# Performance work log

Hardware: AMD Instinct MI355X
Metric: run time of the kernel (lower is better)

## Reference

```python
import jax, jax.numpy as jnp
import numpy as np

NUM_SEQS = 4
SEQ_LEN = 2048
T = NUM_SEQS * SEQ_LEN          # total tokens
D_IN = 4096
D_OUT = 4096
NUM_ADAPTERS = 8
MAX_RANK = 64
CACHE_LEN = NUM_ADAPTERS * MAX_RANK  # 512 pages


def setup_inputs() -> dict:
    key = jax.random.key(0)
    ks = jax.random.split(key, 8)
    x = jax.random.normal(ks[0], (T, D_IN), dtype=jnp.float32)
    weight = jax.random.normal(ks[1], (D_OUT, D_IN), dtype=jnp.float32) * 0.02
    bias = jax.random.normal(ks[2], (D_OUT,), dtype=jnp.float32) * 0.02
    a_cache = jax.random.normal(ks[3], (CACHE_LEN, D_IN), dtype=jnp.float32) * 0.02
    b_cache = jax.random.normal(ks[4], (CACHE_LEN, D_OUT), dtype=jnp.float32) * 0.02
    b_start_loc = (jnp.arange(NUM_SEQS) * SEQ_LEN).astype(jnp.int32)
    b_adapter_ids = jax.random.randint(ks[5], (NUM_SEQS,), 0, NUM_ADAPTERS).astype(jnp.int32)
    b_scaling = jax.random.uniform(ks[6], (NUM_SEQS,), dtype=jnp.float32, minval=0.5, maxval=2.0)
    # page i for (adapter a, rank slot r) lives at a*MAX_RANK + r
    rank_page_table = jnp.arange(CACHE_LEN, dtype=jnp.int32).reshape(NUM_ADAPTERS, MAX_RANK)
    ranks = jax.random.randint(ks[7], (NUM_ADAPTERS,), 1, MAX_RANK + 1).astype(jnp.int32)
    return {"x": x, "weight": weight, "bias": bias, "a_cache": a_cache,
            "b_cache": b_cache, "b_start_loc": b_start_loc,
            "b_adapter_ids": b_adapter_ids, "b_scaling": b_scaling,
            "rank_page_table": rank_page_table, "ranks": ranks}


def reference(x, weight, bias, a_cache, b_cache, b_start_loc,
              b_adapter_ids, b_scaling, rank_page_table, ranks):
    t = x.shape[0]
    num_adapters, max_rank = rank_page_table.shape
    # map each token to its sequence -> adapter id / scaling (mbgmm dispatch)
    seg = jnp.searchsorted(b_start_loc, jnp.arange(t, dtype=b_start_loc.dtype),
                           side='right') - 1                      # [T]
    tok_adapter = b_adapter_ids[seg]                              # [T]
    tok_scale = b_scaling[seg]                                    # [T]
    # gather paged LoRA A/B weights per adapter: [A, R, D]
    A_all = a_cache[rank_page_table]                              # [A, R, D_in]
    B_all = b_cache[rank_page_table]                              # [A, R, D_out]
    # mbgmm_a: xa[t, r] = x[t] . A[adapter(t), r], zero beyond rank
    xa_all = jnp.einsum('td,ard->tar', x, A_all)                  # [T, A, R]
    rmask = (jnp.arange(max_rank)[None, :] < ranks[:, None])      # [A, R]
    onehot = (tok_adapter[:, None] == jnp.arange(num_adapters)[None, :])  # [T, A]
    sel = (onehot[:, :, None] & rmask[None, :, :]).astype(x.dtype)  # [T, A, R]
    xa_sel = xa_all * sel
    # mbgmm_b: lora_out[t] = scaling * sum_r xa[t, r] * B[adapter(t), r]
    lora_out = jnp.einsum('tar,aro->to', xa_sel, B_all) * tok_scale[:, None]
    base_out = x @ weight.T + bias
    return base_out + lora_out
```

## Files before the change

kernel.cpp:

```cpp
#include <hip/hip_runtime.h>
#include <hip/hip_bf16.h>

typedef unsigned short u16;
typedef unsigned int u32;
typedef __attribute__((ext_vector_type(8))) short bf16x8;
typedef __attribute__((ext_vector_type(4))) float f32x4;

#define T_TOK 8192
#define DIN 4096
#define DOUT 4096
#define N_SEQS 4
#define N_ADPT 8
#define MAXR 64
#define CACHE_LEN 512

__device__ __forceinline__ u16 f2bf(float f) {
    u32 u = __builtin_bit_cast(u32, f);
    u += 0x7fffu + ((u >> 16) & 1u);
    return (u16)(u >> 16);
}

__device__ __forceinline__ void load_lds16(const u16* g, u16* l) {
    __builtin_amdgcn_global_load_lds(
        (const __attribute__((address_space(1))) u32*)g,
        (__attribute__((address_space(3))) u32*)l, 16, 0, 0);
}

__global__ void cvt_all(const float* __restrict__ x, const float* __restrict__ w,
                        const float* __restrict__ a,
                        u16* __restrict__ xb, u16* __restrict__ wb, u16* __restrict__ ab) {
    const int n_x = T_TOK * DIN / 4, n_w = DOUT * DIN / 4, n_a = CACHE_LEN * DIN / 4;
    int i = blockIdx.x * 256 + threadIdx.x;
    int stride = gridDim.x * 256;
    for (int j = i; j < n_x + n_w + n_a; j += stride) {
        const float* src; u16* dst; int k;
        if (j < n_x)            { src = x; dst = xb; k = j; }
        else if (j < n_x + n_w) { src = w; dst = wb; k = j - n_x; }
        else                    { src = a; dst = ab; k = j - n_x - n_w; }
        float4 v = reinterpret_cast<const float4*>(src)[k];
        ushort4 o;
        o.x = f2bf(v.x); o.y = f2bf(v.y); o.z = f2bf(v.z); o.w = f2bf(v.w);
        reinterpret_cast<ushort4*>(dst)[k] = o;
    }
}

__global__ void build_bt(const float* __restrict__ b_cache, const int* __restrict__ rpt,
                         u16* __restrict__ Bt) {
    int id = blockIdx.x * 256 + threadIdx.x;
    int n  = id & (DOUT - 1);
    int rb = (id >> 12) & 7;
    int a  = id >> 15;
    union { u16 u[8]; uint4 v; } pack;
    #pragma unroll
    for (int j = 0; j < 8; ++j) {
        int r = rb * 8 + j;
        int page = rpt[a * MAXR + r];
        pack.u[j] = f2bf(b_cache[(long)page * DOUT + n]);
    }
    *reinterpret_cast<uint4*>(&Bt[((long)(a * DOUT + n)) * MAXR + rb * 8]) = pack.v;
}

__launch_bounds__(256)
__global__ void xa_kernel(const u16* __restrict__ xb, const u16* __restrict__ ab,
                          const int* __restrict__ b_start_loc,
                          const int* __restrict__ b_adapter_ids,
                          const int* __restrict__ rpt,
                          float* __restrict__ xa_part) {
    int tblk = blockIdx.x >> 2, kseg = blockIdx.x & 3;
    int t0 = tblk * 128;
    int seg = 0;
    #pragma unroll
    for (int i = 1; i < N_SEQS; ++i) if (b_start_loc[i] <= t0) seg = i;
    int adapter = b_adapter_ids[seg];

    __shared__ __attribute__((aligned(16))) u16 As[2 * 4096];
    __shared__ __attribute__((aligned(16))) u16 Bs[2 * 2048];

    int tid = threadIdx.x;
    int lane = tid & 63, wave = tid >> 6;
    int lr = lane & 15, lk = lane >> 4;

    int e0 = wave * 64 + lane;
    int e1 = 256 + e0;
    int ra0 = e0 >> 2, ca0 = (e0 & 3) * 8;
    int ra1 = e1 >> 2, ca1 = (e1 & 3) * 8;
    const u16* gA0 = xb + (long)(t0 + ra0) * DIN + kseg * 1024 + ca0;
    const u16* gA1 = xb + (long)(t0 + ra1) * DIN + kseg * 1024 + ca1;
    int page = rpt[adapter * MAXR + ra0];
    const u16* gB = ab + (long)page * DIN + kseg * 1024 + ca0;

    f32x4 acc[2][4] = {};

    #define XSTAGE(s, buf)                                                         \
        do {                                                                       \
            load_lds16(gA0 + (s) * 32, As + (buf) * 4096 + wave * 512);            \
            load_lds16(gA1 + (s) * 32, As + (buf) * 4096 + 2048 + wave * 512);     \
            load_lds16(gB + (s) * 32,  Bs + (buf) * 2048 + wave * 512);            \
        } while (0)

    XSTAGE(0, 0);
    for (int s = 0; s < 32; ++s) {
        int b = s & 1;
        if (s < 31) {
            XSTAGE(s + 1, b ^ 1);
            asm volatile("s_waitcnt vmcnt(3)" ::: "memory");
        } else {
            asm volatile("s_waitcnt vmcnt(0)" ::: "memory");
        }
        __builtin_amdgcn_s_barrier();
        __builtin_amdgcn_sched_barrier(0);

        bf16x8 af[2], bfr[4];
        #pragma unroll
        for (int m = 0; m < 2; ++m)
            af[m] = *(const bf16x8*)&As[b * 4096 + (wave * 32 + m * 16 + lr) * 32 + lk * 8];
        #pragma unroll
        for (int n = 0; n < 4; ++n)
            bfr[n] = *(const bf16x8*)&Bs[b * 2048 + (n * 16 + lr) * 32 + lk * 8];
        #pragma unroll
        for (int m = 0; m < 2; ++m)
            #pragma unroll
            for (int n = 0; n < 4; ++n)
                acc[m][n] = __builtin_amdgcn_mfma_f32_16x16x32_bf16(af[m], bfr[n], acc[m][n], 0, 0, 0);

        __builtin_amdgcn_s_barrier();
        __builtin_amdgcn_sched_barrier(0);
    }
    #undef XSTAGE

    float* dst = xa_part + (long)kseg * T_TOK * MAXR;
    #pragma unroll
    for (int m = 0; m < 2; ++m) {
        int trow = t0 + wave * 32 + m * 16 + lk * 4;
        #pragma unroll
        for (int n = 0; n < 4; ++n) {
            int r = n * 16 + lr;
            #pragma unroll
            for (int j = 0; j < 4; ++j)
                dst[(long)(trow + j) * MAXR + r] = acc[m][n][j];
        }
    }
}

__global__ void xa_fin(const float* __restrict__ xa_part,
                       const int* __restrict__ b_start_loc,
                       const int* __restrict__ b_adapter_ids,
                       const float* __restrict__ b_scaling,
                       const int* __restrict__ ranks,
                       u16* __restrict__ xa) {
    const int N = T_TOK * MAXR;
    int i = blockIdx.x * 256 + threadIdx.x;
    if (i >= N) return;
    int t = i >> 6, r = i & 63;
    int seg = 0;
    #pragma unroll
    for (int s = 1; s < N_SEQS; ++s) if (b_start_loc[s] <= t) seg = s;
    int adapter = b_adapter_ids[seg];
    float v = xa_part[i] + xa_part[N + i] + xa_part[2 * N + i] + xa_part[3 * N + i];
    v = (r < ranks[adapter]) ? v * b_scaling[seg] : 0.0f;
    xa[i] = f2bf(v);
}

__launch_bounds__(512, 2)
__global__ void gemm256_kernel(const u16* __restrict__ xb, const u16* __restrict__ wb,
                               const float* __restrict__ bias,
                               const u16* __restrict__ xa, const u16* __restrict__ Bt,
                               const int* __restrict__ b_start_loc,
                               const int* __restrict__ b_adapter_ids,
                               float* __restrict__ out) {
    __shared__ __attribute__((aligned(16))) u16 lds[32768];

    int bid = blockIdx.x;
    int wgid = (bid & 7) * 64 + (bid >> 3);
    int mt = wgid >> 4, nt = wgid & 15;
    int brow = mt * 256, bcol = nt * 256;

    int seg = 0;
    #pragma unroll
    for (int i = 1; i < N_SEQS; ++i) if (b_start_loc[i] <= brow) seg = i;
    int adapter = b_adapter_ids[seg];

    int tid = threadIdx.x;
    int lane = tid & 63, wave = tid >> 6;
    int wm = wave >> 2, wn = wave & 3;
    int lr = lane & 15, lk = lane >> 4;

    int lsw = (tid & 7) ^ ((tid >> 3) & 7);
    int c8  = (lsw & 3) * 8;
    int r0  = (tid >> 3) * 2 + (lsw >> 2);
    const long odA0 = (long)(brow + r0) * DIN + c8;
    const long odA1 = odA0 + 128L * DIN;
    const long odB0 = (long)(bcol + r0) * DIN + c8;
    const long odB1 = odB0 + 128L * DIN;
    const long o6A0 = (long)(brow + r0) * MAXR + c8;
    const long o6A1 = o6A0 + 128L * MAXR;
    const long o6B0 = (long)(adapter * DOUT + bcol + r0) * MAXR + c8;
    const long o6B1 = o6B0 + 128L * MAXR;

    #define STAGE(T, buf)                                                          \
        do {                                                                       \
            u16* dA = lds + (buf) * 8192 + tid * 8;                                \
            u16* dB = lds + 16384 + (buf) * 8192 + tid * 8;                        \
            if ((T) < 128) {                                                       \
                long ko = (long)(T) * 32;                                          \
                load_lds16(xb + odA0 + ko, dA);                                    \
                load_lds16(xb + odA1 + ko, dA + 4096);                             \
                load_lds16(wb + odB0 + ko, dB);                                    \
                load_lds16(wb + odB1 + ko, dB + 4096);                             \
            } else {                                                               \
                long ko = (long)((T) - 128) * 32;                                  \
                load_lds16(xa + o6A0 + ko, dA);                                    \
                load_lds16(xa + o6A1 + ko, dA + 4096);                             \
                load_lds16(Bt + o6B0 + ko, dB);                                    \
                load_lds16(Bt + o6B1 + ko, dB + 4096);                             \
            }                                                                      \
        } while (0)

    const int laneByte = (lr >> 1) * 128 + 16 * ((((lr & 1) << 2) + lk) ^ (lr >> 1));
    const char* ldsc = (const char*)lds;
    const int cA = wm * 8192 + laneByte;
    const int cB = 32768 + wn * 4096 + laneByte;

    #define READF(FA, FB, par)                                                     \
        do {                                                                       \
            const char* pA = ldsc + (par) * 16384 + cA;                            \
            const char* pB = ldsc + (par) * 16384 + cB;                            \
            _Pragma("unroll")                                                      \
            for (int ni = 0; ni < 4; ++ni) FB[ni] = *(const bf16x8*)(pB + ni * 1024); \
            _Pragma("unroll")                                                      \
            for (int mi = 0; mi < 8; ++mi) FA[mi] = *(const bf16x8*)(pA + mi * 1024); \
        } while (0)

    #define MFMA32(FA, FB)                                                         \
        do {                                                                       \
            _Pragma("unroll")                                                      \
            for (int mi = 0; mi < 8; ++mi)                                         \
                _Pragma("unroll")                                                  \
                for (int ni = 0; ni < 4; ++ni)                                     \
                    acc[mi][ni] = __builtin_amdgcn_mfma_f32_16x16x32_bf16(         \
                        FA[mi], FB[ni], acc[mi][ni], 0, 0, 0);                     \
        } while (0)

    #define ENDBAR()                                                               \
        do {                                                                       \
            asm volatile("s_waitcnt lgkmcnt(0)" ::: "memory");                     \
            __builtin_amdgcn_sched_barrier(0);                                     \
            __builtin_amdgcn_s_barrier();                                          \
        } while (0)

    f32x4 acc[8][4] = {};
    bf16x8 fA0[8], fB0[4], fA1[8], fB1[4];

    STAGE(0, 0);
    STAGE(1, 1);
    asm volatile("s_waitcnt vmcnt(4)" ::: "memory");
    __builtin_amdgcn_s_barrier();
    READF(fA0, fB0, 0);
    ENDBAR();

    for (int t = 0; t < 130; t += 2) {
        STAGE((t + 2 < 130) ? t + 2 : 129, t & 1);
        asm volatile("s_waitcnt vmcnt(4)" ::: "memory");
        __builtin_amdgcn_s_barrier();
        READF(fA1, fB1, (t + 1) & 1);
        MFMA32(fA0, fB0);
        ENDBAR();

        STAGE((t + 3 < 130) ? t + 3 : 129, (t + 1) & 1);
        asm volatile("s_waitcnt vmcnt(4)" ::: "memory");
        __builtin_amdgcn_s_barrier();
        if (t + 2 < 130) READF(fA0, fB0, t & 1);
        MFMA32(fA1, fB1);
        ENDBAR();
    }
    asm volatile("s_waitcnt vmcnt(0)" ::: "memory");

    #undef STAGE
    #undef READF
    #undef MFMA32
    #undef ENDBAR

    #pragma unroll
    for (int m = 0; m < 8; ++m) {
        int orow = brow + wm * 128 + m * 16 + lk * 4;
        #pragma unroll
        for (int n = 0; n < 4; ++n) {
            int ocol = bcol + wn * 64 + n * 16 + lr;
            float bv = bias[ocol];
            #pragma unroll
            for (int j = 0; j < 4; ++j)
                out[(long)(orow + j) * DOUT + ocol] = acc[m][n][j] + bv;
        }
    }
}

extern "C" void kernel_launch(void* const* d_in, const int* in_sizes, int n_in,
                              void* d_out, int out_size, void* d_ws, size_t ws_size,
                              hipStream_t stream) {
    const float* x          = (const float*)d_in[0];
    const float* weight     = (const float*)d_in[1];
    const float* bias       = (const float*)d_in[2];
    const float* a_cache    = (const float*)d_in[3];
    const float* b_cache    = (const float*)d_in[4];
    const int*   b_start    = (const int*)d_in[5];
    const int*   b_adapter  = (const int*)d_in[6];
    const float* b_scaling  = (const float*)d_in[7];
    const int*   rpt        = (const int*)d_in[8];
    const int*   ranks      = (const int*)d_in[9];
    float* out = (float*)d_out;

    char* ws = (char*)d_ws;
    u16*   xb      = (u16*)ws;   ws += (size_t)T_TOK * DIN * 2;
    u16*   wb      = (u16*)ws;   ws += (size_t)DOUT * DIN * 2;
    u16*   ab      = (u16*)ws;   ws += (size_t)CACHE_LEN * DIN * 2;
    u16*   Bt      = (u16*)ws;   ws += (size_t)N_ADPT * DOUT * MAXR * 2;
    u16*   xa      = (u16*)ws;   ws += (size_t)T_TOK * MAXR * 2;
    float* xa_part = (float*)ws; ws += (size_t)4 * T_TOK * MAXR * 4;

    cvt_all<<<2048, 256, 0, stream>>>(x, weight, a_cache, xb, wb, ab);
    build_bt<<<(N_ADPT * 8 * DOUT) / 256, 256, 0, stream>>>(b_cache, rpt, Bt);
    xa_kernel<<<(T_TOK / 128) * 4, 256, 0, stream>>>(xb, ab, b_start, b_adapter, rpt, xa_part);
    xa_fin<<<(T_TOK * MAXR + 255) / 256, 256, 0, stream>>>(xa_part, b_start, b_adapter, b_scaling, ranks, xa);
    gemm256_kernel<<<(T_TOK / 256) * (DOUT / 256), 512, 0, stream>>>(xb, wb, bias, xa, Bt, b_start, b_adapter, out);
}
```

Measured before the change: 329.2 us.

## Use 4 waves per 256x256 tile with 128x128 per-wave output

Halves the GEMM workgroup from 512 to 256 threads. Each of the 4 waves now computes a 128x128 sub-tile with 8x8 MFMA accumulators, and each thread issues 8 global-to-LDS loads per stage instead of 4. This raises per-wave data reuse from LDS fragments and cuts barrier participants. In exchange it doubles accumulator registers (256 VGPRs of acc), which risks spills or lower occupancy, and halves the waves available to hide latency.

```diff
diff --git a/kernel.cpp b/kernel.cpp
--- a/kernel.cpp
+++ b/kernel.cpp
@@ -161,7 +161,7 @@
     xa[i] = f2bf(v);
 }
 
-__launch_bounds__(512, 2)
+__launch_bounds__(256, 1)
 __global__ void gemm256_kernel(const u16* __restrict__ xb, const u16* __restrict__ wb,
                                const float* __restrict__ bias,
                                const u16* __restrict__ xa, const u16* __restrict__ Bt,
@@ -182,20 +182,16 @@
 
     int tid = threadIdx.x;
     int lane = tid & 63, wave = tid >> 6;
-    int wm = wave >> 2, wn = wave & 3;
+    int wm = wave >> 1, wn = wave & 1;
     int lr = lane & 15, lk = lane >> 4;
 
     int lsw = (tid & 7) ^ ((tid >> 3) & 7);
     int c8  = (lsw & 3) * 8;
     int r0  = (tid >> 3) * 2 + (lsw >> 2);
     const long odA0 = (long)(brow + r0) * DIN + c8;
-    const long odA1 = odA0 + 128L * DIN;
     const long odB0 = (long)(bcol + r0) * DIN + c8;
-    const long odB1 = odB0 + 128L * DIN;
     const long o6A0 = (long)(brow + r0) * MAXR + c8;
-    const long o6A1 = o6A0 + 128L * MAXR;
     const long o6B0 = (long)(adapter * DOUT + bcol + r0) * MAXR + c8;
-    const long o6B1 = o6B0 + 128L * MAXR;
 
     #define STAGE(T, buf)                                                          \
         do {                                                                       \
@@ -203,40 +199,42 @@
             u16* dB = lds + 16384 + (buf) * 8192 + tid * 8;                        \
             if ((T) < 128) {                                                       \
                 long ko = (long)(T) * 32;                                          \
-                load_lds16(xb + odA0 + ko, dA);                                    \
-                load_lds16(xb + odA1 + ko, dA + 4096);                             \
-                load_lds16(wb + odB0 + ko, dB);                                    \
-                load_lds16(wb + odB1 + ko, dB + 4096);                             \
+                _Pragma("unroll")                                                  \
+                for (int q = 0; q < 4; ++q) {                                      \
+                    load_lds16(xb + odA0 + q * (64L * DIN) + ko, dA + q * 2048);   \
+                    load_lds16(wb + odB0 + q * (64L * DIN) + ko, dB + q * 2048);   \
+                }                                                                  \
             } else {                                                               \
                 long ko = (long)((T) - 128) * 32;                                  \
-                load_lds16(xa + o6A0 + ko, dA);                                    \
-                load_lds16(xa + o6A1 + ko, dA + 4096);                             \
-                load_lds16(Bt + o6B0 + ko, dB);                                    \
-                load_lds16(Bt + o6B1 + ko, dB + 4096);                             \
+                _Pragma("unroll")                                                  \
+                for (int q = 0; q < 4; ++q) {                                      \
+                    load_lds16(xa + o6A0 + q * (64L * MAXR) + ko, dA + q * 2048);  \
+                    load_lds16(Bt + o6B0 + q * (64L * MAXR) + ko, dB + q * 2048);  \
+                }                                                                  \
             }                                                                      \
         } while (0)
 
     const int laneByte = (lr >> 1) * 128 + 16 * ((((lr & 1) << 2) + lk) ^ (lr >> 1));
     const char* ldsc = (const char*)lds;
     const int cA = wm * 8192 + laneByte;
-    const int cB = 32768 + wn * 4096 + laneByte;
+    const int cB = 32768 + wn * 8192 + laneByte;
 
     #define READF(FA, FB, par)                                                     \
         do {                                                                       \
             const char* pA = ldsc + (par) * 16384 + cA;                            \
             const char* pB = ldsc + (par) * 16384 + cB;                            \
             _Pragma("unroll")                                                      \
-            for (int ni = 0; ni < 4; ++ni) FB[ni] = *(const bf16x8*)(pB + ni * 1024); \
+            for (int ni = 0; ni < 8; ++ni) FB[ni] = *(const bf16x8*)(pB + ni * 1024); \
             _Pragma("unroll")                                                      \
             for (int mi = 0; mi < 8; ++mi) FA[mi] = *(const bf16x8*)(pA + mi * 1024); \
         } while (0)
 
-    #define MFMA32(FA, FB)                                                         \
+    #define MFMA64(FA, FB)                                                         \
         do {                                                                       \
             _Pragma("unroll")                                                      \
             for (int mi = 0; mi < 8; ++mi)                                         \
                 _Pragma("unroll")                                                  \
-                for (int ni = 0; ni < 4; ++ni)                                     \
+                for (int ni = 0; ni < 8; ++ni)                                     \
                     acc[mi][ni] = __builtin_amdgcn_mfma_f32_16x16x32_bf16(         \
                         FA[mi], FB[ni], acc[mi][ni], 0, 0, 0);                     \
         } while (0)
@@ -248,44 +246,44 @@
             __builtin_amdgcn_s_barrier();                                          \
         } while (0)
 
-    f32x4 acc[8][4] = {};
-    bf16x8 fA0[8], fB0[4], fA1[8], fB1[4];
+    f32x4 acc[8][8] = {};
+    bf16x8 fA0[8], fB0[8], fA1[8], fB1[8];
 
     STAGE(0, 0);
     STAGE(1, 1);
-    asm volatile("s_waitcnt vmcnt(4)" ::: "memory");
+    asm volatile("s_waitcnt vmcnt(8)" ::: "memory");
     __builtin_amdgcn_s_barrier();
     READF(fA0, fB0, 0);
     ENDBAR();
 
     for (int t = 0; t < 130; t += 2) {
         STAGE((t + 2 < 130) ? t + 2 : 129, t & 1);
-        asm volatile("s_waitcnt vmcnt(4)" ::: "memory");
+        asm volatile("s_waitcnt vmcnt(8)" ::: "memory");
         __builtin_amdgcn_s_barrier();
         READF(fA1, fB1, (t + 1) & 1);
-        MFMA32(fA0, fB0);
+        MFMA64(fA0, fB0);
         ENDBAR();
 
         STAGE((t + 3 < 130) ? t + 3 : 129, (t + 1) & 1);
-        asm volatile("s_waitcnt vmcnt(4)" ::: "memory");
+        asm volatile("s_waitcnt vmcnt(8)" ::: "memory");
         __builtin_amdgcn_s_barrier();
         if (t + 2 < 130) READF(fA0, fB0, t & 1);
-        MFMA32(fA1, fB1);
+        MFMA64(fA1, fB1);
         ENDBAR();
     }
     asm volatile("s_waitcnt vmcnt(0)" ::: "memory");
 
     #undef STAGE
     #undef READF
-    #undef MFMA32
+    #undef MFMA64
     #undef ENDBAR
 
     #pragma unroll
     for (int m = 0; m < 8; ++m) {
         int orow = brow + wm * 128 + m * 16 + lk * 4;
         #pragma unroll
-        for (int n = 0; n < 4; ++n) {
-            int ocol = bcol + wn * 64 + n * 16 + lr;
+        for (int n = 0; n < 8; ++n) {
+            int ocol = bcol + wn * 128 + n * 16 + lr;
             float bv = bias[ocol];
             #pragma unroll
             for (int j = 0; j < 4; ++j)
@@ -321,5 +319,5 @@
     build_bt<<<(N_ADPT * 8 * DOUT) / 256, 256, 0, stream>>>(b_cache, rpt, Bt);
     xa_kernel<<<(T_TOK / 128) * 4, 256, 0, stream>>>(xb, ab, b_start, b_adapter, rpt, xa_part);
     xa_fin<<<(T_TOK * MAXR + 255) / 256, 256, 0, stream>>>(xa_part, b_start, b_adapter, b_scaling, ranks, xa);
-    gemm256_kernel<<<(T_TOK / 256) * (DOUT / 256), 512, 0, stream>>>(xb, wb, bias, xa, Bt, b_start, b_adapter, out);
-}
+    gemm256_kernel<<<(T_TOK / 256) * (DOUT / 256), 256, 0, stream>>>(xb, wb, bias, xa, Bt, b_start, b_adapter, out);
+}
```

Result: slower. 917.7 us (+178.7%).
